# Kernel tuning notes

Hardware: AMD Instinct MI355X
Metric: run time of the kernel (lower is better)

Reference implementation:

```python
import jax, jax.numpy as jnp
import numpy as np

N = 100000
E = 1600000
D_IN, D_HID, D_OUT = 128, 256, 128


def setup_inputs() -> dict:
    key = jax.random.key(0)
    ks = jax.random.split(key, 8)
    x = jax.random.normal(ks[0], (N, D_IN), dtype=jnp.float32)
    edge_index = jax.random.randint(ks[1], (2, E), 0, N, dtype=jnp.int64)
    # PyG SAGEConv params: lin_l (applied to aggregated neighbors, has bias),
    # lin_r (applied to root/self, no bias). Stored as [in, out] for x @ W.
    s0 = 1.0 / np.sqrt(D_IN)
    s1 = 1.0 / np.sqrt(D_HID)
    Wl0 = jax.random.uniform(ks[2], (D_IN, D_HID), jnp.float32, -s0, s0)
    bl0 = jnp.zeros((D_HID,), jnp.float32)
    Wr0 = jax.random.uniform(ks[3], (D_IN, D_HID), jnp.float32, -s0, s0)
    Wl1 = jax.random.uniform(ks[4], (D_HID, D_OUT), jnp.float32, -s1, s1)
    bl1 = jnp.zeros((D_OUT,), jnp.float32)
    Wr1 = jax.random.uniform(ks[5], (D_HID, D_OUT), jnp.float32, -s1, s1)
    return {"x": x, "edge_index": edge_index, "Wl0": Wl0, "bl0": bl0,
            "Wr0": Wr0, "Wl1": Wl1, "bl1": bl1, "Wr1": Wr1}


def _sage_conv(x, src, dst, W_l, b_l, W_r, num_nodes):
    # mean-aggregate source features at destination nodes
    msg = x[src]                                         # [E, d] gather
    agg = jax.ops.segment_sum(msg, dst, num_segments=num_nodes)  # [N, d]
    deg = jax.ops.segment_sum(jnp.ones((src.shape[0],), x.dtype), dst,
                              num_segments=num_nodes)    # [N]
    agg = agg / jnp.maximum(deg, 1.0)[:, None]
    return agg @ W_l + b_l + x @ W_r                     # [N, out]


def reference(x, edge_index, Wl0, bl0, Wr0, Wl1, bl1, Wr1):
    src, dst = edge_index[0], edge_index[1]
    n = x.shape[0]
    h = _sage_conv(x, src, dst, Wl0, bl0, Wr0, n)
    h = jax.nn.relu(h)  # dropout is identity in eval mode
    out = _sage_conv(h, src, dst, Wl1, bl1, Wr1, n)
    return out
```

## Files before the change

kernel.cpp:

```cpp
#include <hip/hip_runtime.h>

typedef short bf16x8 __attribute__((ext_vector_type(8)));
typedef float f32x4 __attribute__((ext_vector_type(4)));
typedef unsigned int uint;
typedef unsigned short ushort;
typedef ushort u16x8 __attribute__((ext_vector_type(8)));
typedef uint u32x2 __attribute__((ext_vector_type(2)));
typedef uint u32x4 __attribute__((ext_vector_type(4)));

#define NBLK 256
#define LCAP 24576

__device__ inline ushort f2bf(float f) {
    uint u = __builtin_bit_cast(uint, f);
    uint r = u + 0x7fffu + ((u >> 16) & 1u);
    return (ushort)(r >> 16);
}
__device__ inline float bf2f(uint lo16) {
    uint u = lo16 << 16;
    return __builtin_bit_cast(float, u);
}
__device__ inline float bf2f_hi(uint v) {
    uint u = v & 0xffff0000u;
    return __builtin_bit_cast(float, u);
}

__device__ inline void packw_body(const float* __restrict__ Wa, const float* __restrict__ Wb,
                                  ushort* __restrict__ out, int mode, int tile, int l) {
    int cb = tile >> 3, ks = tile & 7;
    int col = cb * 16 + (l & 15);
    int k0 = ks * 32 + ((l >> 4) * 8);
    ushort vals[8];
#pragma unroll
    for (int j = 0; j < 8; j++) {
        int k = k0 + j;
        float f;
        if (mode == 0)
            f = (k < 128) ? Wa[(size_t)k * 256 + col] : Wb[(size_t)(k - 128) * 256 + col];
        else
            f = (col < 128) ? Wa[(size_t)k * 128 + col] : Wb[(size_t)k * 128 + (col - 128)];
        vals[j] = f2bf(f);
    }
    ushort* dst = out + ((size_t)tile * 64 + l) * 8;
#pragma unroll
    for (int j = 0; j < 8; j++) dst[j] = vals[j];
}

__global__ void prep_kernel(const float* __restrict__ x, ushort* __restrict__ a1,
                            const float* __restrict__ Wr0, const float* __restrict__ Wl0,
                            ushort* __restrict__ w1p,
                            const float* __restrict__ Wl1, const float* __restrict__ Wr1,
                            ushort* __restrict__ w2p,
                            const int* __restrict__ dst, int* __restrict__ ghist,
                            int E, int CE, int NB, int n) {
    __shared__ int hist[512];
    int bb = blockIdx.x;
    int tid = threadIdx.x;
    if (bb < NBLK) {
        for (int b = tid; b < NB; b += 256) hist[b] = 0;
        __syncthreads();
        int start = bb * CE, end = min(E, start + CE);
        for (int e = start + tid; e < end; e += 256) {
            int d = dst[e];
            atomicAdd(&hist[d >> 8], 1);
        }
        __syncthreads();
        for (int b = tid; b < NB; b += 256) ghist[(size_t)b * NBLK + bb] = hist[b];
    } else if (bb < NBLK + 64) {
        int r = bb - NBLK;
        int tile = (r & 31) * 4 + (tid >> 6);
        int l = tid & 63;
        if (r < 32) packw_body(Wr0, Wl0, w1p, 0, tile, l);
        else        packw_body(Wl1, Wr1, w2p, 1, tile, l);
    } else {
        int i = (bb - NBLK - 64) * 256 + tid;
        int total = n * 32;
        if (i < total) {
            int row = i >> 5, q = i & 31;
            float4 v = *(const float4*)(x + (size_t)row * 128 + q * 4);
            ushort4 o;
            o.x = f2bf(v.x); o.y = f2bf(v.y); o.z = f2bf(v.z); o.w = f2bf(v.w);
            *(ushort4*)(a1 + (size_t)row * 256 + q * 4) = o;
        }
    }
}

__global__ void scan1_kernel(const int* __restrict__ cnt, int* __restrict__ rs,
                             int* __restrict__ bsum, int n) {
    __shared__ int tmp[256];
    int tid = threadIdx.x;
    int idx = blockIdx.x * 256 + tid;
    int v = (idx < n) ? cnt[idx] : 0;
    tmp[tid] = v;
    __syncthreads();
#pragma unroll
    for (int off = 1; off < 256; off <<= 1) {
        int t = (tid >= off) ? tmp[tid - off] : 0;
        __syncthreads();
        tmp[tid] += t;
        __syncthreads();
    }
    if (idx < n) rs[idx] = tmp[tid] - v;
    if (tid == 255) bsum[blockIdx.x] = tmp[255];
}

__global__ void scan23_kernel(int* __restrict__ rs, const int* __restrict__ bsum,
                              int n, int E) {
    __shared__ int red[256];
    int tid = threadIdx.x;
    int b = blockIdx.x;
    int s = 0;
    for (int t = tid; t < b; t += 256) s += bsum[t];
    red[tid] = s;
    __syncthreads();
#pragma unroll
    for (int off = 128; off > 0; off >>= 1) {
        if (tid < off) red[tid] += red[tid + off];
        __syncthreads();
    }
    int offv = red[0];
    int idx = b * 256 + tid;
    if (idx < n) rs[idx] += offv;
    if (b == 0 && tid == 0) rs[n] = E;
}

__global__ void p3_kernel(const int* __restrict__ src, const int* __restrict__ dst,
                          const int* __restrict__ goff, uint* __restrict__ ebuck,
                          int E, int CE, int NB) {
    __shared__ int cur[512];
    int tid = threadIdx.x;
    for (int b = tid; b < NB; b += 256) cur[b] = goff[(size_t)b * NBLK + blockIdx.x];
    __syncthreads();
    int start = blockIdx.x * CE, end = min(E, start + CE);
    for (int e = start + tid; e < end; e += 256) {
        int d = dst[e];
        int s = src[e];
        int slot = atomicAdd(&cur[d >> 8], 1);
        ebuck[slot] = ((uint)(d & 255) << 17) | (uint)s;
    }
}

__global__ void p4_kernel(const uint* __restrict__ ebuck, const int* __restrict__ goff,
                          int* __restrict__ rs, int* __restrict__ nbr, int n, int E, int NB) {
    __shared__ uint ebuf[LCAP];
    __shared__ int cnt[256];
    __shared__ int cur[256];
    int tid = threadIdx.x;
    int b = blockIdx.x;
    int d0 = b << 8;
    int eb = goff[(size_t)b * NBLK];
    int ee = (b == NB - 1) ? E : goff[(size_t)(b + 1) * NBLK];
    cnt[tid] = 0;
    __syncthreads();
    int m = ee - eb;
    for (int i = tid; i < m; i += 256) {
        uint v = ebuck[eb + i];
        if (i < LCAP) ebuf[i] = v;
        atomicAdd(&cnt[v >> 17], 1);
    }
    __syncthreads();
    int v0 = cnt[tid];
    cur[tid] = v0;
    __syncthreads();
#pragma unroll
    for (int off = 1; off < 256; off <<= 1) {
        int t = (tid >= off) ? cur[tid - off] : 0;
        __syncthreads();
        cur[tid] += t;
        __syncthreads();
    }
    int excl = cur[tid] - v0;
    int node = d0 + tid;
    if (node < n) rs[node] = eb + excl;
    if (b == NB - 1 && tid == 0) rs[n] = E;
    __syncthreads();
    cur[tid] = eb + excl;
    __syncthreads();
    for (int i = tid; i < m; i += 256) {
        uint v = (i < LCAP) ? ebuf[i] : ebuck[eb + i];
        int p = atomicAdd(&cur[v >> 17], 1);
        nbr[p] = (int)(v & 0x1FFFFu);
    }
}

template <int LAYER>
__launch_bounds__(256, 2)
__global__ void mfma_gemm_kernel(const ushort* __restrict__ A, const ushort* __restrict__ Wp,
                                 const float* __restrict__ bias, ushort* __restrict__ out_bf,
                                 float* __restrict__ out_f, int n) {
    __shared__ unsigned char smem[65536];
    int tid = threadIdx.x;
    int l = tid & 63, w = tid >> 6;
    int row0 = blockIdx.x * 128 + w * 32;

    bf16x8 a[2][8];
#pragma unroll
    for (int g = 0; g < 2; g++) {
        int ar = row0 + g * 16 + (l & 15);
        if (ar > n - 1) ar = n - 1;
        const ushort* ap = A + (size_t)ar * 256 + ((l >> 4) * 8);
#pragma unroll
        for (int ks = 0; ks < 8; ks++) a[g][ks] = *(const bf16x8*)(ap + ks * 32);
    }

    f32x4 acc[2][16];
#pragma unroll
    for (int g = 0; g < 2; g++)
#pragma unroll
        for (int cb = 0; cb < 16; cb++) acc[g][cb] = (f32x4){0.f, 0.f, 0.f, 0.f};

    const unsigned char* wbytes = (const unsigned char*)Wp;

#pragma unroll
    for (int half = 0; half < 2; half++) {
        {
            const unsigned char* src = wbytes + half * 65536;
#pragma unroll
            for (int i = 0; i < 16; i += 4) {
                u32x4 t0 = *(const u32x4*)(src + (size_t)(i + 0) * 4096 + tid * 16);
                u32x4 t1 = *(const u32x4*)(src + (size_t)(i + 1) * 4096 + tid * 16);
                u32x4 t2 = *(const u32x4*)(src + (size_t)(i + 2) * 4096 + tid * 16);
                u32x4 t3 = *(const u32x4*)(src + (size_t)(i + 3) * 4096 + tid * 16);
                *(u32x4*)(smem + (i + 0) * 4096 + tid * 16) = t0;
                *(u32x4*)(smem + (i + 1) * 4096 + tid * 16) = t1;
                *(u32x4*)(smem + (i + 2) * 4096 + tid * 16) = t2;
                *(u32x4*)(smem + (i + 3) * 4096 + tid * 16) = t3;
            }
        }
        __syncthreads();
#pragma unroll
        for (int cb = 0; cb < 8; cb++) {
            bf16x8 b[8];
            const unsigned char* bp = smem + ((size_t)(cb * 8) * 64 + l) * 16;
#pragma unroll
            for (int ks = 0; ks < 8; ks++) b[ks] = *(const bf16x8*)(bp + (size_t)ks * 1024);
#pragma unroll
            for (int ks = 0; ks < 8; ks++) {
                acc[0][half * 8 + cb] =
                    __builtin_amdgcn_mfma_f32_16x16x32_bf16(b[ks], a[0][ks], acc[0][half * 8 + cb], 0, 0, 0);
                acc[1][half * 8 + cb] =
                    __builtin_amdgcn_mfma_f32_16x16x32_bf16(b[ks], a[1][ks], acc[1][half * 8 + cb], 0, 0, 0);
            }
        }
        __syncthreads();
    }

    if (LAYER == 0) {
        ushort* ep = (ushort*)(void*)smem + (size_t)w * (16 * 272);
#pragma unroll
        for (int g = 0; g < 2; g++) {
            int rbase = row0 + g * 16;
#pragma unroll
            for (int cb = 0; cb < 16; cb++) {
                int colb = cb * 16 + (l >> 4) * 4;
                f32x4 bv = *(const f32x4*)(bias + colb);
                f32x4 v = acc[g][cb];
                float v0 = fmaxf(v[0] + bv[0], 0.f);
                float v1 = fmaxf(v[1] + bv[1], 0.f);
                float v2 = fmaxf(v[2] + bv[2], 0.f);
                float v3 = fmaxf(v[3] + bv[3], 0.f);
                u32x2 pk;
                pk[0] = (uint)f2bf(v0) | ((uint)f2bf(v1) << 16);
                pk[1] = (uint)f2bf(v2) | ((uint)f2bf(v3) << 16);
                *(u32x2*)&ep[(l & 15) * 272 + colb] = pk;
            }
            int rr = l >> 2, q = l & 3;
            int row = rbase + rr;
#pragma unroll
            for (int rep = 0; rep < 8; rep++) {
                u16x8 vv = *(const u16x8*)&ep[rr * 272 + q * 8 + rep * 32];
                if (row < n)
                    *(u16x8*)(out_bf + (size_t)row * 256 + q * 8 + rep * 32) = vv;
            }
        }
    } else {
        ushort* ep = (ushort*)(void*)smem + (size_t)w * (16 * 136);
#pragma unroll
        for (int g = 0; g < 2; g++) {
            int rbase = row0 + g * 16;
#pragma unroll
            for (int cb = 0; cb < 8; cb++) {
                int colb = cb * 16 + (l >> 4) * 4;
                f32x4 v = acc[g][cb];
                u32x2 pk;
                pk[0] = (uint)f2bf(v[0]) | ((uint)f2bf(v[1]) << 16);
                pk[1] = (uint)f2bf(v[2]) | ((uint)f2bf(v[3]) << 16);
                *(u32x2*)&ep[(l & 15) * 136 + colb] = pk;
            }
            {
                int rr = l >> 2, q = l & 3;
                int row = rbase + rr;
#pragma unroll
                for (int rep = 0; rep < 4; rep++) {
                    u16x8 vv = *(const u16x8*)&ep[rr * 136 + q * 8 + rep * 32];
                    if (row < n)
                        *(u16x8*)(out_bf + (size_t)row * 128 + q * 8 + rep * 32) = vv;
                }
            }
            int orow = rbase + (l & 15);
#pragma unroll
            for (int cb = 8; cb < 16; cb++) {
                int colb = (cb - 8) * 16 + (l >> 4) * 4;
                f32x4 bv = *(const f32x4*)(bias + colb);
                f32x4 v = acc[g][cb];
                v[0] += bv[0]; v[1] += bv[1]; v[2] += bv[2]; v[3] += bv[3];
                if (orow < n)
                    *(f32x4*)(out_f + (size_t)orow * 128 + colb) = v;
            }
        }
    }
}

template <int ADD>
__global__ void segmean_kernel(const uint* __restrict__ fp, int half ,
                               const int* __restrict__ rs, const int* __restrict__ nbr,
                               uint* __restrict__ outb, float* __restrict__ outf, int n) {
    int w = threadIdx.x >> 6;
    int l = threadIdx.x & 63;
    int i = blockIdx.x * 4 + w;
    if (i >= n) return;
    int b = rs[i], e = rs[i + 1];
    int q = l & 31;
    int hsel = l >> 5;
    int stride2 = half >> 1;
    const uint2* fpq = (const uint2*)fp + q;
    float a0 = 0.f, a1 = 0.f, a2 = 0.f, a3 = 0.f;
    int j = b;
    for (; j + 8 <= e; j += 8) {
        int s[4];
#pragma unroll
        for (int p = 0; p < 4; p++) s[p] = nbr[j + 2 * p + hsel];
        uint2 v[4];
#pragma unroll
        for (int p = 0; p < 4; p++) v[p] = fpq[(size_t)s[p] * stride2];
#pragma unroll
        for (int p = 0; p < 4; p++) {
            a0 += bf2f(v[p].x & 0xffffu); a1 += bf2f_hi(v[p].x);
            a2 += bf2f(v[p].y & 0xffffu); a3 += bf2f_hi(v[p].y);
        }
    }
    for (; j + 2 <= e; j += 2) {
        int s = nbr[j + hsel];
        uint2 v = fpq[(size_t)s * stride2];
        a0 += bf2f(v.x & 0xffffu); a1 += bf2f_hi(v.x);
        a2 += bf2f(v.y & 0xffffu); a3 += bf2f_hi(v.y);
    }
    if (j < e && hsel == 0) {
        int s = nbr[j];
        uint2 v = fpq[(size_t)s * stride2];
        a0 += bf2f(v.x & 0xffffu); a1 += bf2f_hi(v.x);
        a2 += bf2f(v.y & 0xffffu); a3 += bf2f_hi(v.y);
    }
    a0 += __shfl_xor(a0, 32);
    a1 += __shfl_xor(a1, 32);
    a2 += __shfl_xor(a2, 32);
    a3 += __shfl_xor(a3, 32);
    if (hsel == 0) {
        int dg = e - b;
        float inv = 1.0f / (float)(dg > 1 ? dg : 1);
        a0 *= inv; a1 *= inv; a2 *= inv; a3 *= inv;
        if (ADD) {
            float* op = outf + (size_t)i * (2 * half) + q * 4;
            f32x4 o = *(const f32x4*)op;
            o[0] += a0; o[1] += a1; o[2] += a2; o[3] += a3;
            *(f32x4*)op = o;
        } else {
            u32x2 pk;
            pk[0] = (uint)f2bf(a0) | ((uint)f2bf(a1) << 16);
            pk[1] = (uint)f2bf(a2) | ((uint)f2bf(a3) << 16);
            *(u32x2*)(outb + (size_t)i * half + q * 2) = pk;
        }
    }
}


extern "C" void kernel_launch(void* const* d_in, const int* in_sizes, int n_in,
                              void* d_out, int out_size, void* d_ws, size_t ws_size,
                              hipStream_t stream) {
    const float* x = (const float*)d_in[0];
    const int* ei = (const int*)d_in[1];
    const float* Wl0 = (const float*)d_in[2];
    const float* bl0 = (const float*)d_in[3];
    const float* Wr0 = (const float*)d_in[4];
    const float* Wl1 = (const float*)d_in[5];
    const float* bl1 = (const float*)d_in[6];
    const float* Wr1 = (const float*)d_in[7];
    float* outp = (float*)d_out;

    int n = in_sizes[0] / 128;
    int E = in_sizes[1] / 2;
    const int* srcv = ei;
    const int* dstv = ei + E;

    int NB = (n + 255) >> 8;
    int NG = NB * NBLK;
    int CE = (E + NBLK - 1) / NBLK;

    char* w = (char*)d_ws;
    auto align = [](size_t v) { return (v + 255) & ~(size_t)255; };
    size_t off = 0;
    int* rs    = (int*)(w + off); off = align(off + (size_t)(n + 1) * 4);
    int* bsum2 = (int*)(w + off); off = align(off + (size_t)512 * 4);
    int* ghist = (int*)(w + off); off = align(off + (size_t)(NG + 1) * 4);
    int* goff  = (int*)(w + off); off = align(off + (size_t)(NG + 1) * 4);
    uint* ebuck = (uint*)(w + off); off = align(off + (size_t)E * 4);
    int* nbr   = (int*)(w + off); off = align(off + (size_t)E * 4);
    ushort* a1  = (ushort*)(w + off); off = align(off + (size_t)n * 256 * 2);
    ushort* hb  = (ushort*)(w + off); off = align(off + (size_t)n * 256 * 2);
    ushort* zb  = (ushort*)(w + off); off = align(off + (size_t)n * 128 * 2);
    ushort* w1p = (ushort*)(w + off); off = align(off + (size_t)256 * 256 * 2);
    ushort* w2p = (ushort*)(w + off); off = align(off + (size_t)256 * 256 * 2);
    (void)ws_size; (void)n_in; (void)out_size;

    int nb2 = (NG + 255) / 256;
    int ncx = (n * 32 + 255) / 256;

    prep_kernel<<<NBLK + 64 + ncx, 256, 0, stream>>>(x, a1, Wr0, Wl0, w1p, Wl1, Wr1, w2p,
                                                     dstv, ghist, E, CE, NB, n);
    scan1_kernel<<<nb2, 256, 0, stream>>>(ghist, goff, bsum2, NG);
    scan23_kernel<<<nb2, 256, 0, stream>>>(goff, bsum2, NG, E);
    p3_kernel<<<NBLK, 256, 0, stream>>>(srcv, dstv, goff, ebuck, E, CE, NB);
    p4_kernel<<<NB, 256, 0, stream>>>(ebuck, goff, rs, nbr, n, E, NB);

    int segb = (n + 3) / 4;
    int mb = (n + 127) / 128;

    segmean_kernel<0><<<segb, 256, 0, stream>>>((const uint*)a1, 128, rs, nbr,
                                                (uint*)(a1 + 128), nullptr, n);
    mfma_gemm_kernel<0><<<mb, 256, 0, stream>>>(a1, w1p, bl0, hb, nullptr, n);

    mfma_gemm_kernel<1><<<mb, 256, 0, stream>>>(hb, w2p, bl1, zb, outp, n);
    segmean_kernel<1><<<segb, 256, 0, stream>>>((const uint*)zb, 64, rs, nbr,
                                                nullptr, outp, n);
}
```

Measured before the change: 266.6 us.

## Fuse both layer GEMMs into one kernel keeping hidden activations in LDS

Merges the two dense GEMM kernels into one. Each block stages its 128-row input tile in LDS, computes the first layer with bias and ReLU, writes the bf16 hidden tile back into LDS, then runs the second-layer GEMM from it. This removes the global write and re-read of the N×256 bf16 hidden buffer plus one kernel launch. In exchange it uses about 130 KB of dynamic LDS at occupancy 1, repacks the weights by k-slice, and adds more synchronisation and LDS traffic per block.

After: 272.9 us. 1.02x slower.

```diff
diff --git a/kernel.cpp b/kernel.cpp
--- a/kernel.cpp
+++ b/kernel.cpp
@@ -10,6 +10,7 @@
 
 #define NBLK 256
 #define LCAP 24576
+#define HP 264
 
 __device__ inline ushort f2bf(float f) {
     uint u = __builtin_bit_cast(uint, f);
@@ -41,7 +42,7 @@
             f = (col < 128) ? Wa[(size_t)k * 128 + col] : Wb[(size_t)k * 128 + (col - 128)];
         vals[j] = f2bf(f);
     }
-    ushort* dst = out + ((size_t)tile * 64 + l) * 8;
+    ushort* dst = out + ((size_t)(ks * 16 + cb) * 64 + l) * 8;
 #pragma unroll
     for (int j = 0; j < 8; j++) dst[j] = vals[j];
 }
@@ -183,25 +184,31 @@
     }
 }
 
-template <int LAYER>
-__launch_bounds__(256, 2)
-__global__ void mfma_gemm_kernel(const ushort* __restrict__ A, const ushort* __restrict__ Wp,
-                                 const float* __restrict__ bias, ushort* __restrict__ out_bf,
-                                 float* __restrict__ out_f, int n) {
-    __shared__ unsigned char smem[65536];
+__launch_bounds__(256, 1)
+__global__ void fused_gemm_kernel(const ushort* __restrict__ A, const ushort* __restrict__ W1,
+                                  const ushort* __restrict__ W2, const float* __restrict__ b0,
+                                  const float* __restrict__ b1, ushort* __restrict__ zb,
+                                  float* __restrict__ outf, int n) {
+    extern __shared__ unsigned char smem[];
+    unsigned char* regW = smem;
+    ushort* H = (ushort*)(smem + 65536);
     int tid = threadIdx.x;
     int l = tid & 63, w = tid >> 6;
-    int row0 = blockIdx.x * 128 + w * 32;
-
-    bf16x8 a[2][8];
-#pragma unroll
-    for (int g = 0; g < 2; g++) {
-        int ar = row0 + g * 16 + (l & 15);
-        if (ar > n - 1) ar = n - 1;
-        const ushort* ap = A + (size_t)ar * 256 + ((l >> 4) * 8);
-#pragma unroll
-        for (int ks = 0; ks < 8; ks++) a[g][ks] = *(const bf16x8*)(ap + ks * 32);
-    }
+    int row0 = blockIdx.x * 128;
+
+    {
+        int r = tid >> 5;
+        int c = (tid & 31) * 8;
+#pragma unroll
+        for (int it = 0; it < 16; it++) {
+            int lr = it * 8 + r;
+            int row = row0 + lr;
+            if (row > n - 1) row = n - 1;
+            u32x4 v = *(const u32x4*)(A + (size_t)row * 256 + c);
+            *(u32x4*)(H + (size_t)lr * HP + c) = v;
+        }
+    }
+    __syncthreads();
 
     f32x4 acc[2][16];
 #pragma unroll
@@ -209,110 +216,148 @@
 #pragma unroll
         for (int cb = 0; cb < 16; cb++) acc[g][cb] = (f32x4){0.f, 0.f, 0.f, 0.f};
 
-    const unsigned char* wbytes = (const unsigned char*)Wp;
+    int arow = w * 32 + (l & 15);
+    int acol = (l >> 4) * 8;
 
 #pragma unroll
     for (int half = 0; half < 2; half++) {
         {
-            const unsigned char* src = wbytes + half * 65536;
+            const unsigned char* src = (const unsigned char*)W1 + half * 65536;
 #pragma unroll
             for (int i = 0; i < 16; i += 4) {
                 u32x4 t0 = *(const u32x4*)(src + (size_t)(i + 0) * 4096 + tid * 16);
                 u32x4 t1 = *(const u32x4*)(src + (size_t)(i + 1) * 4096 + tid * 16);
                 u32x4 t2 = *(const u32x4*)(src + (size_t)(i + 2) * 4096 + tid * 16);
                 u32x4 t3 = *(const u32x4*)(src + (size_t)(i + 3) * 4096 + tid * 16);
-                *(u32x4*)(smem + (i + 0) * 4096 + tid * 16) = t0;
-                *(u32x4*)(smem + (i + 1) * 4096 + tid * 16) = t1;
-                *(u32x4*)(smem + (i + 2) * 4096 + tid * 16) = t2;
-                *(u32x4*)(smem + (i + 3) * 4096 + tid * 16) = t3;
+                *(u32x4*)(regW + (i + 0) * 4096 + tid * 16) = t0;
+                *(u32x4*)(regW + (i + 1) * 4096 + tid * 16) = t1;
+                *(u32x4*)(regW + (i + 2) * 4096 + tid * 16) = t2;
+                *(u32x4*)(regW + (i + 3) * 4096 + tid * 16) = t3;
             }
         }
-        __syncthreads();
+        bf16x8 a[2][4];
+#pragma unroll
+        for (int g = 0; g < 2; g++)
+#pragma unroll
+            for (int ksl = 0; ksl < 4; ksl++)
+                a[g][ksl] = *(const bf16x8*)(H + (size_t)(arow + g * 16) * HP +
+                                             (half * 4 + ksl) * 32 + acol);
+        __syncthreads();
+#pragma unroll
+        for (int cb = 0; cb < 16; cb++) {
+            bf16x8 b[4];
+#pragma unroll
+            for (int ksl = 0; ksl < 4; ksl++)
+                b[ksl] = *(const bf16x8*)(regW + ((size_t)(ksl * 16 + cb) * 64 + l) * 16);
+#pragma unroll
+            for (int ksl = 0; ksl < 4; ksl++) {
+                acc[0][cb] = __builtin_amdgcn_mfma_f32_16x16x32_bf16(b[ksl], a[0][ksl], acc[0][cb], 0, 0, 0);
+                acc[1][cb] = __builtin_amdgcn_mfma_f32_16x16x32_bf16(b[ksl], a[1][ksl], acc[1][cb], 0, 0, 0);
+            }
+        }
+        __syncthreads();
+    }
+
+#pragma unroll
+    for (int g = 0; g < 2; g++) {
+        int lr = arow + g * 16;
+#pragma unroll
+        for (int cb = 0; cb < 16; cb++) {
+            int colb = cb * 16 + (l >> 4) * 4;
+            f32x4 bv = *(const f32x4*)(b0 + colb);
+            f32x4 v = acc[g][cb];
+            float v0 = fmaxf(v[0] + bv[0], 0.f);
+            float v1 = fmaxf(v[1] + bv[1], 0.f);
+            float v2 = fmaxf(v[2] + bv[2], 0.f);
+            float v3 = fmaxf(v[3] + bv[3], 0.f);
+            u32x2 pk;
+            pk[0] = (uint)f2bf(v0) | ((uint)f2bf(v1) << 16);
+            pk[1] = (uint)f2bf(v2) | ((uint)f2bf(v3) << 16);
+            *(u32x2*)(H + (size_t)lr * HP + colb) = pk;
+        }
+    }
+#pragma unroll
+    for (int g = 0; g < 2; g++)
+#pragma unroll
+        for (int cb = 0; cb < 16; cb++) acc[g][cb] = (f32x4){0.f, 0.f, 0.f, 0.f};
+
+#pragma unroll
+    for (int half = 0; half < 2; half++) {
+        {
+            const unsigned char* src = (const unsigned char*)W2 + half * 65536;
+#pragma unroll
+            for (int i = 0; i < 16; i += 4) {
+                u32x4 t0 = *(const u32x4*)(src + (size_t)(i + 0) * 4096 + tid * 16);
+                u32x4 t1 = *(const u32x4*)(src + (size_t)(i + 1) * 4096 + tid * 16);
+                u32x4 t2 = *(const u32x4*)(src + (size_t)(i + 2) * 4096 + tid * 16);
+                u32x4 t3 = *(const u32x4*)(src + (size_t)(i + 3) * 4096 + tid * 16);
+                *(u32x4*)(regW + (i + 0) * 4096 + tid * 16) = t0;
+                *(u32x4*)(regW + (i + 1) * 4096 + tid * 16) = t1;
+                *(u32x4*)(regW + (i + 2) * 4096 + tid * 16) = t2;
+                *(u32x4*)(regW + (i + 3) * 4096 + tid * 16) = t3;
+            }
+        }
+        bf16x8 a[2][4];
+#pragma unroll
+        for (int g = 0; g < 2; g++)
+#pragma unroll
+            for (int ksl = 0; ksl < 4; ksl++)
+                a[g][ksl] = *(const bf16x8*)(H + (size_t)(arow + g * 16) * HP +
+                                             (half * 4 + ksl) * 32 + acol);
+        __syncthreads();
+#pragma unroll
+        for (int cb = 0; cb < 16; cb++) {
+            bf16x8 b[4];
+#pragma unroll
+            for (int ksl = 0; ksl < 4; ksl++)
+                b[ksl] = *(const bf16x8*)(regW + ((size_t)(ksl * 16 + cb) * 64 + l) * 16);
+#pragma unroll
+            for (int ksl = 0; ksl < 4; ksl++) {
+                acc[0][cb] = __builtin_amdgcn_mfma_f32_16x16x32_bf16(b[ksl], a[0][ksl], acc[0][cb], 0, 0, 0);
+                acc[1][cb] = __builtin_amdgcn_mfma_f32_16x16x32_bf16(b[ksl], a[1][ksl], acc[1][cb], 0, 0, 0);
+            }
+        }
+        __syncthreads();
+    }
+
+    ushort* ep = H + (size_t)w * (16 * 136);
+#pragma unroll
+    for (int g = 0; g < 2; g++) {
+        int rbase = row0 + w * 32 + g * 16;
 #pragma unroll
         for (int cb = 0; cb < 8; cb++) {
-            bf16x8 b[8];
-            const unsigned char* bp = smem + ((size_t)(cb * 8) * 64 + l) * 16;
-#pragma unroll
-            for (int ks = 0; ks < 8; ks++) b[ks] = *(const bf16x8*)(bp + (size_t)ks * 1024);
-#pragma unroll
-            for (int ks = 0; ks < 8; ks++) {
-                acc[0][half * 8 + cb] =
-                    __builtin_amdgcn_mfma_f32_16x16x32_bf16(b[ks], a[0][ks], acc[0][half * 8 + cb], 0, 0, 0);
-                acc[1][half * 8 + cb] =
-                    __builtin_amdgcn_mfma_f32_16x16x32_bf16(b[ks], a[1][ks], acc[1][half * 8 + cb], 0, 0, 0);
-            }
-        }
-        __syncthreads();
-    }
-
-    if (LAYER == 0) {
-        ushort* ep = (ushort*)(void*)smem + (size_t)w * (16 * 272);
-#pragma unroll
-        for (int g = 0; g < 2; g++) {
-            int rbase = row0 + g * 16;
-#pragma unroll
-            for (int cb = 0; cb < 16; cb++) {
-                int colb = cb * 16 + (l >> 4) * 4;
-                f32x4 bv = *(const f32x4*)(bias + colb);
-                f32x4 v = acc[g][cb];
-                float v0 = fmaxf(v[0] + bv[0], 0.f);
-                float v1 = fmaxf(v[1] + bv[1], 0.f);
-                float v2 = fmaxf(v[2] + bv[2], 0.f);
-                float v3 = fmaxf(v[3] + bv[3], 0.f);
-                u32x2 pk;
-                pk[0] = (uint)f2bf(v0) | ((uint)f2bf(v1) << 16);
-                pk[1] = (uint)f2bf(v2) | ((uint)f2bf(v3) << 16);
-                *(u32x2*)&ep[(l & 15) * 272 + colb] = pk;
-            }
+            int colb = cb * 16 + (l >> 4) * 4;
+            f32x4 v = acc[g][cb];
+            u32x2 pk;
+            pk[0] = (uint)f2bf(v[0]) | ((uint)f2bf(v[1]) << 16);
+            pk[1] = (uint)f2bf(v[2]) | ((uint)f2bf(v[3]) << 16);
+            *(u32x2*)&ep[(l & 15) * 136 + colb] = pk;
+        }
+        {
             int rr = l >> 2, q = l & 3;
             int row = rbase + rr;
 #pragma unroll
-            for (int rep = 0; rep < 8; rep++) {
-                u16x8 vv = *(const u16x8*)&ep[rr * 272 + q * 8 + rep * 32];
+            for (int rep = 0; rep < 4; rep++) {
+                u16x8 vv = *(const u16x8*)&ep[rr * 136 + q * 8 + rep * 32];
                 if (row < n)
-                    *(u16x8*)(out_bf + (size_t)row * 256 + q * 8 + rep * 32) = vv;
+                    *(u16x8*)(zb + (size_t)row * 128 + q * 8 + rep * 32) = vv;
             }
         }
-    } else {
-        ushort* ep = (ushort*)(void*)smem + (size_t)w * (16 * 136);
-#pragma unroll
-        for (int g = 0; g < 2; g++) {
-            int rbase = row0 + g * 16;
-#pragma unroll
-            for (int cb = 0; cb < 8; cb++) {
-                int colb = cb * 16 + (l >> 4) * 4;
-                f32x4 v = acc[g][cb];
-                u32x2 pk;
-                pk[0] = (uint)f2bf(v[0]) | ((uint)f2bf(v[1]) << 16);
-                pk[1] = (uint)f2bf(v[2]) | ((uint)f2bf(v[3]) << 16);
-                *(u32x2*)&ep[(l & 15) * 136 + colb] = pk;
-            }
-            {
-                int rr = l >> 2, q = l & 3;
-                int row = rbase + rr;
-#pragma unroll
-                for (int rep = 0; rep < 4; rep++) {
-                    u16x8 vv = *(const u16x8*)&ep[rr * 136 + q * 8 + rep * 32];
-                    if (row < n)
-                        *(u16x8*)(out_bf + (size_t)row * 128 + q * 8 + rep * 32) = vv;
-                }
-            }
-            int orow = rbase + (l & 15);
-#pragma unroll
-            for (int cb = 8; cb < 16; cb++) {
-                int colb = (cb - 8) * 16 + (l >> 4) * 4;
-                f32x4 bv = *(const f32x4*)(bias + colb);
-                f32x4 v = acc[g][cb];
-                v[0] += bv[0]; v[1] += bv[1]; v[2] += bv[2]; v[3] += bv[3];
-                if (orow < n)
-                    *(f32x4*)(out_f + (size_t)orow * 128 + colb) = v;
-            }
+        int orow = rbase + (l & 15);
+#pragma unroll
+        for (int cb = 8; cb < 16; cb++) {
+            int colb = (cb - 8) * 16 + (l >> 4) * 4;
+            f32x4 bv = *(const f32x4*)(b1 + colb);
+            f32x4 v = acc[g][cb];
+            v[0] += bv[0]; v[1] += bv[1]; v[2] += bv[2]; v[3] += bv[3];
+            if (orow < n)
+                *(f32x4*)(outf + (size_t)orow * 128 + colb) = v;
         }
     }
 }
 
 template <int ADD>
-__global__ void segmean_kernel(const uint* __restrict__ fp, int half ,
+__global__ void segmean_kernel(const uint* __restrict__ fp, int half,
                                const int* __restrict__ rs, const int* __restrict__ nbr,
                                uint* __restrict__ outb, float* __restrict__ outf, int n) {
     int w = threadIdx.x >> 6;
@@ -406,7 +451,6 @@
     uint* ebuck = (uint*)(w + off); off = align(off + (size_t)E * 4);
     int* nbr   = (int*)(w + off); off = align(off + (size_t)E * 4);
     ushort* a1  = (ushort*)(w + off); off = align(off + (size_t)n * 256 * 2);
-    ushort* hb  = (ushort*)(w + off); off = align(off + (size_t)n * 256 * 2);
     ushort* zb  = (ushort*)(w + off); off = align(off + (size_t)n * 128 * 2);
     ushort* w1p = (ushort*)(w + off); off = align(off + (size_t)256 * 256 * 2);
     ushort* w2p = (ushort*)(w + off); off = align(off + (size_t)256 * 256 * 2);
@@ -424,12 +468,14 @@
 
     int segb = (n + 3) / 4;
     int mb = (n + 127) / 128;
+    int ldsz = 65536 + 128 * HP * 2;
+
+    hipFuncSetAttribute((const void*)fused_gemm_kernel,
+                        hipFuncAttributeMaxDynamicSharedMemorySize, ldsz);
 
     segmean_kernel<0><<<segb, 256, 0, stream>>>((const uint*)a1, 128, rs, nbr,
                                                 (uint*)(a1 + 128), nullptr, n);
-    mfma_gemm_kernel<0><<<mb, 256, 0, stream>>>(a1, w1p, bl0, hb, nullptr, n);
-
-    mfma_gemm_kernel<1><<<mb, 256, 0, stream>>>(hb, w2p, bl1, zb, outp, n);
+    fused_gemm_kernel<<<mb, 256, ldsz, stream>>>(a1, w1p, w2p, bl0, bl1, zb, outp, n);
     segmean_kernel<1><<<segb, 256, 0, stream>>>((const uint*)zb, 64, rs, nbr,
                                                 nullptr, outp, n);
 }
```

## Fuse both layer GEMMs into one kernel keeping hidden activations in LDS

Applied to the files above, without the earlier changes.

Replaces the two per-layer MFMA GEMM kernels with one 512-thread kernel. Each wave computes a 16-row tile of the first layer, writes the ReLU'd bf16 hidden rows to LDS, and reuses them as the A operand for the second layer. This removes the global write and re-read of the N×256 hidden buffer and one kernel launch. Weights are streamed into LDS in four 64 KB chunks with register prefetch of the next chunk, which needed a new packed weight layout. The cost is one block per CU with about 130 KB of LDS, plus an extra barrier pair per chunk.

After: 256.5 us. -3.8%, faster.

```diff
diff --git a/kernel.cpp b/kernel.cpp
--- a/kernel.cpp
+++ b/kernel.cpp
@@ -10,6 +10,7 @@
 
 #define NBLK 256
 #define LCAP 24576
+#define HP 264
 
 __device__ inline ushort f2bf(float f) {
     uint u = __builtin_bit_cast(uint, f);
@@ -41,7 +42,7 @@
             f = (col < 128) ? Wa[(size_t)k * 128 + col] : Wb[(size_t)k * 128 + (col - 128)];
         vals[j] = f2bf(f);
     }
-    ushort* dst = out + ((size_t)tile * 64 + l) * 8;
+    ushort* dst = out + ((size_t)(ks * 16 + cb) * 64 + l) * 8;
 #pragma unroll
     for (int j = 0; j < 8; j++) dst[j] = vals[j];
 }
@@ -183,78 +184,73 @@
     }
 }
 
-template <int LAYER>
-__launch_bounds__(256, 2)
-__global__ void mfma_gemm_kernel(const ushort* __restrict__ A, const ushort* __restrict__ Wp,
-                                 const float* __restrict__ bias, ushort* __restrict__ out_bf,
-                                 float* __restrict__ out_f, int n) {
-    __shared__ unsigned char smem[65536];
+__launch_bounds__(512, 1)
+__global__ void fused_gemm_kernel(const ushort* __restrict__ A, const ushort* __restrict__ W1,
+                                  const ushort* __restrict__ W2, const float* __restrict__ b0,
+                                  const float* __restrict__ b1, ushort* __restrict__ zb,
+                                  float* __restrict__ outf, int n) {
+    extern __shared__ unsigned char smem[];
+    unsigned char* regW = smem;
+    ushort* H = (ushort*)(smem + 65536);
     int tid = threadIdx.x;
     int l = tid & 63, w = tid >> 6;
-    int row0 = blockIdx.x * 128 + w * 32;
-
-    bf16x8 a[2][8];
-#pragma unroll
-    for (int g = 0; g < 2; g++) {
-        int ar = row0 + g * 16 + (l & 15);
-        if (ar > n - 1) ar = n - 1;
-        const ushort* ap = A + (size_t)ar * 256 + ((l >> 4) * 8);
-#pragma unroll
-        for (int ks = 0; ks < 8; ks++) a[g][ks] = *(const bf16x8*)(ap + ks * 32);
-    }
-
-    f32x4 acc[2][16];
-#pragma unroll
-    for (int g = 0; g < 2; g++)
-#pragma unroll
-        for (int cb = 0; cb < 16; cb++) acc[g][cb] = (f32x4){0.f, 0.f, 0.f, 0.f};
-
-    const unsigned char* wbytes = (const unsigned char*)Wp;
-
-#pragma unroll
-    for (int half = 0; half < 2; half++) {
-        {
-            const unsigned char* src = wbytes + half * 65536;
-#pragma unroll
-            for (int i = 0; i < 16; i += 4) {
-                u32x4 t0 = *(const u32x4*)(src + (size_t)(i + 0) * 4096 + tid * 16);
-                u32x4 t1 = *(const u32x4*)(src + (size_t)(i + 1) * 4096 + tid * 16);
-                u32x4 t2 = *(const u32x4*)(src + (size_t)(i + 2) * 4096 + tid * 16);
-                u32x4 t3 = *(const u32x4*)(src + (size_t)(i + 3) * 4096 + tid * 16);
-                *(u32x4*)(smem + (i + 0) * 4096 + tid * 16) = t0;
-                *(u32x4*)(smem + (i + 1) * 4096 + tid * 16) = t1;
-                *(u32x4*)(smem + (i + 2) * 4096 + tid * 16) = t2;
-                *(u32x4*)(smem + (i + 3) * 4096 + tid * 16) = t3;
+    int q = l >> 4;
+    int row0 = blockIdx.x * 128;
+    int lrow16 = l & 15;
+    int grow = row0 + w * 16 + lrow16;
+    if (grow > n - 1) grow = n - 1;
+    ushort* hpriv = H + (size_t)w * (16 * HP);
+
+    const unsigned char* wsrc0 = (const unsigned char*)W1;
+    const unsigned char* wsrc1 = (const unsigned char*)W1 + 65536;
+    const unsigned char* wsrc2 = (const unsigned char*)W2;
+    const unsigned char* wsrc3 = (const unsigned char*)W2 + 65536;
+
+    bf16x8 a[8];
+    {
+        const ushort* ap = A + (size_t)grow * 256 + q * 8;
+#pragma unroll
+        for (int ks = 0; ks < 8; ks++) a[ks] = *(const bf16x8*)(ap + ks * 32);
+    }
+    u32x4 wr[8];
+#pragma unroll
+    for (int i = 0; i < 8; i++) wr[i] = *(const u32x4*)(wsrc0 + (size_t)i * 8192 + tid * 16);
+#pragma unroll
+    for (int i = 0; i < 8; i++) *(u32x4*)(regW + i * 8192 + tid * 16) = wr[i];
+
+    f32x4 acc[16];
+#pragma unroll
+    for (int cb = 0; cb < 16; cb++) acc[cb] = (f32x4){0.f, 0.f, 0.f, 0.f};
+
+    __syncthreads();
+
+#pragma unroll
+    for (int c = 0; c < 4; c++) {
+        if (c == 0) {
+#pragma unroll
+            for (int i = 0; i < 8; i++) wr[i] = *(const u32x4*)(wsrc1 + (size_t)i * 8192 + tid * 16);
+        } else if (c == 1) {
+#pragma unroll
+            for (int i = 0; i < 8; i++) wr[i] = *(const u32x4*)(wsrc2 + (size_t)i * 8192 + tid * 16);
+        } else if (c == 2) {
+#pragma unroll
+            for (int i = 0; i < 8; i++) wr[i] = *(const u32x4*)(wsrc3 + (size_t)i * 8192 + tid * 16);
+        }
+        int hb = c & 1;
+#pragma unroll
+        for (int cb = 0; cb < 16; cb++) {
+#pragma unroll
+            for (int ksl = 0; ksl < 4; ksl++) {
+                bf16x8 b = *(const bf16x8*)(regW + ((size_t)(ksl * 16 + cb) * 64 + l) * 16);
+                acc[cb] = __builtin_amdgcn_mfma_f32_16x16x32_bf16(b, a[hb * 4 + ksl], acc[cb], 0, 0, 0);
             }
         }
-        __syncthreads();
-#pragma unroll
-        for (int cb = 0; cb < 8; cb++) {
-            bf16x8 b[8];
-            const unsigned char* bp = smem + ((size_t)(cb * 8) * 64 + l) * 16;
-#pragma unroll
-            for (int ks = 0; ks < 8; ks++) b[ks] = *(const bf16x8*)(bp + (size_t)ks * 1024);
-#pragma unroll
-            for (int ks = 0; ks < 8; ks++) {
-                acc[0][half * 8 + cb] =
-                    __builtin_amdgcn_mfma_f32_16x16x32_bf16(b[ks], a[0][ks], acc[0][half * 8 + cb], 0, 0, 0);
-                acc[1][half * 8 + cb] =
-                    __builtin_amdgcn_mfma_f32_16x16x32_bf16(b[ks], a[1][ks], acc[1][half * 8 + cb], 0, 0, 0);
-            }
-        }
-        __syncthreads();
-    }
-
-    if (LAYER == 0) {
-        ushort* ep = (ushort*)(void*)smem + (size_t)w * (16 * 272);
-#pragma unroll
-        for (int g = 0; g < 2; g++) {
-            int rbase = row0 + g * 16;
+        if (c == 1) {
 #pragma unroll
             for (int cb = 0; cb < 16; cb++) {
-                int colb = cb * 16 + (l >> 4) * 4;
-                f32x4 bv = *(const f32x4*)(bias + colb);
-                f32x4 v = acc[g][cb];
+                int colb = cb * 16 + q * 4;
+                f32x4 bv = *(const f32x4*)(b0 + colb);
+                f32x4 v = acc[cb];
                 float v0 = fmaxf(v[0] + bv[0], 0.f);
                 float v1 = fmaxf(v[1] + bv[1], 0.f);
                 float v2 = fmaxf(v[2] + bv[2], 0.f);
@@ -262,57 +258,56 @@
                 u32x2 pk;
                 pk[0] = (uint)f2bf(v0) | ((uint)f2bf(v1) << 16);
                 pk[1] = (uint)f2bf(v2) | ((uint)f2bf(v3) << 16);
-                *(u32x2*)&ep[(l & 15) * 272 + colb] = pk;
+                *(u32x2*)(hpriv + (size_t)lrow16 * HP + colb) = pk;
             }
-            int rr = l >> 2, q = l & 3;
-            int row = rbase + rr;
-#pragma unroll
-            for (int rep = 0; rep < 8; rep++) {
-                u16x8 vv = *(const u16x8*)&ep[rr * 272 + q * 8 + rep * 32];
-                if (row < n)
-                    *(u16x8*)(out_bf + (size_t)row * 256 + q * 8 + rep * 32) = vv;
-            }
-        }
-    } else {
-        ushort* ep = (ushort*)(void*)smem + (size_t)w * (16 * 136);
-#pragma unroll
-        for (int g = 0; g < 2; g++) {
-            int rbase = row0 + g * 16;
-#pragma unroll
-            for (int cb = 0; cb < 8; cb++) {
-                int colb = cb * 16 + (l >> 4) * 4;
-                f32x4 v = acc[g][cb];
-                u32x2 pk;
-                pk[0] = (uint)f2bf(v[0]) | ((uint)f2bf(v[1]) << 16);
-                pk[1] = (uint)f2bf(v[2]) | ((uint)f2bf(v[3]) << 16);
-                *(u32x2*)&ep[(l & 15) * 136 + colb] = pk;
-            }
-            {
-                int rr = l >> 2, q = l & 3;
-                int row = rbase + rr;
-#pragma unroll
-                for (int rep = 0; rep < 4; rep++) {
-                    u16x8 vv = *(const u16x8*)&ep[rr * 136 + q * 8 + rep * 32];
-                    if (row < n)
-                        *(u16x8*)(out_bf + (size_t)row * 128 + q * 8 + rep * 32) = vv;
-                }
-            }
-            int orow = rbase + (l & 15);
-#pragma unroll
-            for (int cb = 8; cb < 16; cb++) {
-                int colb = (cb - 8) * 16 + (l >> 4) * 4;
-                f32x4 bv = *(const f32x4*)(bias + colb);
-                f32x4 v = acc[g][cb];
-                v[0] += bv[0]; v[1] += bv[1]; v[2] += bv[2]; v[3] += bv[3];
-                if (orow < n)
-                    *(f32x4*)(out_f + (size_t)orow * 128 + colb) = v;
-            }
-        }
+#pragma unroll
+            for (int ks = 0; ks < 8; ks++)
+                a[ks] = *(const bf16x8*)(hpriv + (size_t)lrow16 * HP + ks * 32 + q * 8);
+#pragma unroll
+            for (int cb = 0; cb < 16; cb++) acc[cb] = (f32x4){0.f, 0.f, 0.f, 0.f};
+        }
+        __syncthreads();
+        if (c < 3) {
+#pragma unroll
+            for (int i = 0; i < 8; i++) *(u32x4*)(regW + i * 8192 + tid * 16) = wr[i];
+        }
+        __syncthreads();
+    }
+
+    int rbase = row0 + w * 16;
+#pragma unroll
+    for (int cb = 0; cb < 8; cb++) {
+        int colb = cb * 16 + q * 4;
+        f32x4 v = acc[cb];
+        u32x2 pk;
+        pk[0] = (uint)f2bf(v[0]) | ((uint)f2bf(v[1]) << 16);
+        pk[1] = (uint)f2bf(v[2]) | ((uint)f2bf(v[3]) << 16);
+        *(u32x2*)&hpriv[lrow16 * 136 + colb] = pk;
+    }
+    {
+        int rr = l >> 2, qq = l & 3;
+        int row = rbase + rr;
+#pragma unroll
+        for (int rep = 0; rep < 4; rep++) {
+            u16x8 vv = *(const u16x8*)&hpriv[rr * 136 + qq * 8 + rep * 32];
+            if (row < n)
+                *(u16x8*)(zb + (size_t)row * 128 + qq * 8 + rep * 32) = vv;
+        }
+    }
+    int orow = rbase + lrow16;
+#pragma unroll
+    for (int cb = 8; cb < 16; cb++) {
+        int colb = (cb - 8) * 16 + q * 4;
+        f32x4 bv = *(const f32x4*)(b1 + colb);
+        f32x4 v = acc[cb];
+        v[0] += bv[0]; v[1] += bv[1]; v[2] += bv[2]; v[3] += bv[3];
+        if (orow < n)
+            *(f32x4*)(outf + (size_t)orow * 128 + colb) = v;
     }
 }
 
 template <int ADD>
-__global__ void segmean_kernel(const uint* __restrict__ fp, int half ,
+__global__ void segmean_kernel(const uint* __restrict__ fp, int half,
                                const int* __restrict__ rs, const int* __restrict__ nbr,
                                uint* __restrict__ outb, float* __restrict__ outf, int n) {
     int w = threadIdx.x >> 6;
@@ -406,7 +401,6 @@
     uint* ebuck = (uint*)(w + off); off = align(off + (size_t)E * 4);
     int* nbr   = (int*)(w + off); off = align(off + (size_t)E * 4);
     ushort* a1  = (ushort*)(w + off); off = align(off + (size_t)n * 256 * 2);
-    ushort* hb  = (ushort*)(w + off); off = align(off + (size_t)n * 256 * 2);
     ushort* zb  = (ushort*)(w + off); off = align(off + (size_t)n * 128 * 2);
     ushort* w1p = (ushort*)(w + off); off = align(off + (size_t)256 * 256 * 2);
     ushort* w2p = (ushort*)(w + off); off = align(off + (size_t)256 * 256 * 2);
@@ -424,12 +418,14 @@
 
     int segb = (n + 3) / 4;
     int mb = (n + 127) / 128;
+    int ldsz = 65536 + 8 * 16 * HP * 2;
+
+    hipFuncSetAttribute((const void*)fused_gemm_kernel,
+                        hipFuncAttributeMaxDynamicSharedMemorySize, ldsz);
 
     segmean_kernel<0><<<segb, 256, 0, stream>>>((const uint*)a1, 128, rs, nbr,
                                                 (uint*)(a1 + 128), nullptr, n);
-    mfma_gemm_kernel<0><<<mb, 256, 0, stream>>>(a1, w1p, bl0, hb, nullptr, n);
-
-    mfma_gemm_kernel<1><<<mb, 256, 0, stream>>>(hb, w2p, bl1, zb, outp, n);
+    fused_gemm_kernel<<<mb, 512, ldsz, stream>>>(a1, w1p, w2p, bl0, bl1, zb, outp, n);
     segmean_kernel<1><<<segb, 256, 0, stream>>>((const uint*)zb, 64, rs, nbr,
                                                 nullptr, outp, n);
 }
```
